# Kernel tuning notes

Measured on AMD Instinct MI355X. Metric: run time of the kernel, lower is better.

## Reference

```python
import jax, jax.numpy as jnp
import numpy as np

TAU = 2.0
THETA_BASE = 0.5
SURROGATE_ALPHA = 4.0


def setup_inputs() -> dict:
    key = jax.random.key(0)
    x = jax.random.normal(key, (1024, 32, 1024), dtype=jnp.float32)  # (T, B, F)
    return {"x": x}


def reference(x):
    # Linear recurrence I[t] = decay * I[t-1] + x[t], I[-1] = 0,
    # solved with a log-depth associative scan (matches forward_parallel /
    # matmul_recursive in the torch module, and forward(use_deer=True)).
    decay = jnp.exp(jnp.asarray(-1.0 / TAU, dtype=x.dtype))
    a = jnp.full_like(x, decay)  # per-step decay coefficient

    def combine(c1, c2):
        a1, b1 = c1
        a2, b2 = c2
        return (a1 * a2, a2 * b1 + b2)

    _, I = jax.lax.associative_scan(combine, (a, x), axis=0)  # (T, B, F)
    # Surrogate sigmoid spike (used in both train and eval per _compute_spikes_adaptive)
    spike = jax.nn.sigmoid(SURROGATE_ALPHA * (I - THETA_BASE))
    return spike
```

## Files before the change

kernel.cpp:

```cpp
#include <hip/hip_runtime.h>


#define T_DIM   1024
#define B_DIM   32
#define F_DIM   1024
#define LCHUNK  16
#define KHALO   16
#define F4_DIM  (F_DIM / 4)
#define SEQ4    (B_DIM * F4_DIM)
#define NCHUNK  (T_DIM / LCHUNK)
#define G       8

typedef float f32x4 __attribute__((ext_vector_type(4)));

__device__ __forceinline__ float spike1(float I) {
    float z = fmaf(-4.0f, I, 2.0f);
    float e = __expf(z);
    return __builtin_amdgcn_rcpf(1.0f + e);
}

__device__ __forceinline__ f32x4 spike4(f32x4 I) {
    f32x4 r;
    r.x = spike1(I.x); r.y = spike1(I.y); r.z = spike1(I.z); r.w = spike1(I.w);
    return r;
}

__global__ __launch_bounds__(256, 6) void lif_scan_kernel(
        const f32x4* __restrict__ x, f32x4* __restrict__ out) {
    const float d = 0.60653065971263342f;

    int tid   = blockIdx.x * 256 + threadIdx.x;
    int s     = tid & (SEQ4 - 1);
    int chunk = tid >> 13;
    int t0    = chunk * LCHUNK;

    f32x4 I = (f32x4)(0.0f);
    f32x4 a[G], b[G];

    if (t0 == 0) {
        #pragma unroll
        for (int j = 0; j < G; ++j) a[j] = x[s + j * SEQ4];
        #pragma unroll
        for (int j = 0; j < G; ++j) b[j] = x[s + (G + j) * SEQ4];
        #pragma unroll
        for (int j = 0; j < G; ++j) {
            I = d * I + a[j];
            out[s + j * SEQ4] = spike4(I);
        }
        #pragma unroll
        for (int j = 0; j < G; ++j) {
            I = d * I + b[j];
            out[s + (G + j) * SEQ4] = spike4(I);
        }
    } else {
        int li = (t0 - KHALO) * SEQ4 + s;
        #pragma unroll
        for (int j = 0; j < G; ++j) a[j] = x[li + j * SEQ4];
        #pragma unroll
        for (int j = 0; j < G; ++j) b[j] = x[li + (G + j) * SEQ4];

        #pragma unroll
        for (int j = 0; j < G; ++j) I = d * I + a[j];
        #pragma unroll
        for (int j = 0; j < G; ++j) a[j] = x[li + (2 * G + j) * SEQ4];
        #pragma unroll
        for (int j = 0; j < G; ++j) I = d * I + b[j];
        #pragma unroll
        for (int j = 0; j < G; ++j) b[j] = x[li + (3 * G + j) * SEQ4];

        int si = t0 * SEQ4 + s;
        #pragma unroll
        for (int j = 0; j < G; ++j) {
            I = d * I + a[j];
            out[si + j * SEQ4] = spike4(I);
        }
        #pragma unroll
        for (int j = 0; j < G; ++j) {
            I = d * I + b[j];
            out[si + (G + j) * SEQ4] = spike4(I);
        }
    }
}

extern "C" void kernel_launch(void* const* d_in, const int* in_sizes, int n_in,
                              void* d_out, int out_size, void* d_ws, size_t ws_size,
                              hipStream_t stream) {
    const f32x4* x   = (const f32x4*)d_in[0];
    f32x4*       out = (f32x4*)d_out;
    int total_threads = NCHUNK * SEQ4;
    dim3 grid(total_threads / 256), block(256);
    lif_scan_kernel<<<grid, block, 0, stream>>>(x, out);
}
```

Measured before the change: 230.5 us.

## Double chunk length to cut halo reads, pipeline loads, use nontemporal stores

Raises the time-chunk length from 16 to 32 steps while keeping the 16-step halo, so each thread does twice the output work and redundant halo reads fall from half of all loads to a third. Loads of the next 8-step group are interleaved with the scan-and-store of the current one to keep memory requests in flight. Output stores become nontemporal to avoid cache pollution. The grid halves, which reduces parallelism, and each thread runs a longer serial dependency chain.

```diff
diff --git a/kernel.cpp b/kernel.cpp
--- a/kernel.cpp
+++ b/kernel.cpp
@@ -4,7 +4,7 @@
 #define T_DIM   1024
 #define B_DIM   32
 #define F_DIM   1024
-#define LCHUNK  16
+#define LCHUNK  32
 #define KHALO   16
 #define F4_DIM  (F_DIM / 4)
 #define SEQ4    (B_DIM * F4_DIM)
@@ -25,6 +25,26 @@
     return r;
 }
 
+__device__ __forceinline__ void load8(const f32x4* __restrict__ x,
+                                      f32x4 (&buf)[G], int base) {
+    #pragma unroll
+    for (int j = 0; j < G; ++j) buf[j] = x[base + j * SEQ4];
+}
+
+__device__ __forceinline__ void fma8(f32x4 (&buf)[G], f32x4& I, float d) {
+    #pragma unroll
+    for (int j = 0; j < G; ++j) I = d * I + buf[j];
+}
+
+__device__ __forceinline__ void fmastore8(f32x4 (&buf)[G], f32x4& I, float d,
+                                          f32x4* __restrict__ out, int base) {
+    #pragma unroll
+    for (int j = 0; j < G; ++j) {
+        I = d * I + buf[j];
+        __builtin_nontemporal_store(spike4(I), &out[base + j * SEQ4]);
+    }
+}
+
 __global__ __launch_bounds__(256, 6) void lif_scan_kernel(
         const f32x4* __restrict__ x, f32x4* __restrict__ out) {
     const float d = 0.60653065971263342f;
@@ -36,49 +56,35 @@
 
     f32x4 I = (f32x4)(0.0f);
     f32x4 a[G], b[G];
+    const int GS = G * SEQ4;
 
     if (t0 == 0) {
-        #pragma unroll
-        for (int j = 0; j < G; ++j) a[j] = x[s + j * SEQ4];
-        #pragma unroll
-        for (int j = 0; j < G; ++j) b[j] = x[s + (G + j) * SEQ4];
-        #pragma unroll
-        for (int j = 0; j < G; ++j) {
-            I = d * I + a[j];
-            out[s + j * SEQ4] = spike4(I);
-        }
-        #pragma unroll
-        for (int j = 0; j < G; ++j) {
-            I = d * I + b[j];
-            out[s + (G + j) * SEQ4] = spike4(I);
-        }
+        int li = s;
+        load8(x, a, li); li += GS;
+        load8(x, b, li); li += GS;
+        int si = s;
+        fmastore8(a, I, d, out, si);
+        load8(x, a, li); li += GS;
+        fmastore8(b, I, d, out, si + GS);
+        load8(x, b, li);
+        fmastore8(a, I, d, out, si + 2 * GS);
+        fmastore8(b, I, d, out, si + 3 * GS);
     } else {
         int li = (t0 - KHALO) * SEQ4 + s;
-        #pragma unroll
-        for (int j = 0; j < G; ++j) a[j] = x[li + j * SEQ4];
-        #pragma unroll
-        for (int j = 0; j < G; ++j) b[j] = x[li + (G + j) * SEQ4];
-
-        #pragma unroll
-        for (int j = 0; j < G; ++j) I = d * I + a[j];
-        #pragma unroll
-        for (int j = 0; j < G; ++j) a[j] = x[li + (2 * G + j) * SEQ4];
-        #pragma unroll
-        for (int j = 0; j < G; ++j) I = d * I + b[j];
-        #pragma unroll
-        for (int j = 0; j < G; ++j) b[j] = x[li + (3 * G + j) * SEQ4];
+        load8(x, a, li); li += GS;
+        load8(x, b, li); li += GS;
+        fma8(a, I, d);
+        load8(x, a, li); li += GS;
+        fma8(b, I, d);
+        load8(x, b, li); li += GS;
 
         int si = t0 * SEQ4 + s;
-        #pragma unroll
-        for (int j = 0; j < G; ++j) {
-            I = d * I + a[j];
-            out[si + j * SEQ4] = spike4(I);
-        }
-        #pragma unroll
-        for (int j = 0; j < G; ++j) {
-            I = d * I + b[j];
-            out[si + (G + j) * SEQ4] = spike4(I);
-        }
+        fmastore8(a, I, d, out, si);
+        load8(x, a, li); li += GS;
+        fmastore8(b, I, d, out, si + GS);
+        load8(x, b, li);
+        fmastore8(a, I, d, out, si + 2 * GS);
+        fmastore8(b, I, d, out, si + 3 * GS);
     }
 }
 
```

Result: slower. 241.3 us (+4.7%).
